# Kernel optimization log

Hardware: AMD Instinct MI355X
Metric: run time of the kernel (lower is better)

## Reference

```python
import jax, jax.numpy as jnp
import numpy as np

K_NEIGHBORS = 16  # n_sample

# Each Conv1x1+BatchNorm (eval mode) stage is an exact per-channel affine map,
# so it is represented by a single fused (W, b) pair: y = W @ x + b.

def affine(W, b, x):
    # W: [Cout, Cin]; x: [B, Cin, N] or [B, Cin, N, K]
    if x.ndim == 3:
        return jnp.einsum('oc,bcn->bon', W, x) + b[None, :, None]
    return jnp.einsum('oc,bcnk->bonk', W, x) + b[None, :, None, None]

def knn_idx(p, k):
    # p: [B, N, 3] -> idx of k nearest neighbors (incl. self): [B, N, k]
    sq = jnp.sum(p * p, axis=-1)  # [B, N]
    d2 = sq[:, :, None] + sq[:, None, :] - 2.0 * jnp.einsum('bnc,bmc->bnm', p, p)
    _, idx = jax.lax.top_k(-d2, k)
    return idx

def group(feat, idx):
    # feat: [B, C, N], idx: [B, N, K] -> grouped[b,c,n,k] = feat[b,c,idx[b,n,k]]
    return jax.vmap(lambda f, i: f[:, i])(feat, idx)


def setup_inputs() -> dict:
    key = jax.random.key(0)
    B, C, N = 4, 128, 4096
    ks = jax.random.split(key, 22)
    def w(k, o, i):
        return (jax.random.normal(k, (o, i), jnp.float32) / np.sqrt(i)).astype(jnp.float32)
    def bv(k, o):
        return (jax.random.normal(k, (o,), jnp.float32) * 0.01).astype(jnp.float32)
    inp = {
        'input_p': jax.random.normal(ks[0], (B, 3, N), jnp.float32),
        'input_x': jax.random.normal(ks[1], (B, C, N), jnp.float32),
        'top_W': w(ks[2], C, C),   'top_b': bv(ks[3], C),
        'down_W': w(ks[4], C, C),  'down_b': bv(ks[5], C),
        'phi_W': w(ks[6], C, C),   'phi_b': bv(ks[7], C),
        'psi_W': w(ks[8], C, C),   'psi_b': bv(ks[9], C),
        'alpha_W': w(ks[10], C, C), 'alpha_b': bv(ks[11], C),
        'g1_W': w(ks[12], C, C),   'g1_b': bv(ks[13], C),
        'g2_W': w(ks[14], C, C),   'g2_b': bv(ks[15], C),
        'd1_W': w(ks[16], C, 3),   'd1_b': bv(ks[17], C),
        'd2_W': w(ks[18], C, C),   'd2_b': bv(ks[19], C),
        'a': 0, 'b': 0,
    }
    return inp


def reference(input_p, input_x, top_W, top_b, down_W, down_b, phi_W, phi_b,
              psi_W, psi_b, alpha_W, alpha_b, g1_W, g1_b, g2_W, g2_b,
              d1_W, d1_b, d2_W, d2_b, a, b):
    res = input_x
    p = jnp.transpose(input_p, (0, 2, 1))          # [B, N, 3]
    idx = knn_idx(p, K_NEIGHBORS)                  # [B, N, K]
    grouped_p = group(input_p, idx)                # [B, 3, N, K]
    x = affine(top_W, top_b, input_x)              # linear_top
    phi = affine(phi_W, phi_b, x)[:, :, :, None]   # [B, C, N, 1] (broadcast over K)
    psi = group(affine(psi_W, psi_b, x), idx)      # [B, C, N, K]
    alp = group(affine(alpha_W, alpha_b, x), idx)  # [B, C, N, K]
    rel = input_p[:, :, :, None] - grouped_p       # relative xyz [B, 3, N, K]
    pos = affine(d2_W, d2_b, jax.nn.relu(affine(d1_W, d1_b, rel)))   # delta MLP
    attn = affine(g2_W, g2_b, jax.nn.relu(affine(g1_W, g1_b, phi - psi + pos)))  # gamma MLP
    y = (jax.nn.softmax(attn, axis=-1) * (alp + pos)).sum(axis=-1)   # [B, C, N]
    y = affine(down_W, down_b, y)                  # linear_down
    return y + res
```

## Files before the change

kernel.cpp:

```cpp
#include <hip/hip_runtime.h>
#include <hip/hip_bf16.h>

#define BB 4
#define CC 128
#define NN 4096
#define KK 16
#define FLT_BIG 3.402823466e+38f

typedef __attribute__((ext_vector_type(8))) short short8v;
typedef __attribute__((ext_vector_type(4))) short short4v;
typedef __attribute__((ext_vector_type(4))) float f32x4;

__device__ __forceinline__ unsigned short f2b(float x) {
  union { float f; unsigned u; } v; v.f = x;
  unsigned r = v.u + 0x7fffu + ((v.u >> 16) & 1u);
  return (unsigned short)(r >> 16);
}
__device__ __forceinline__ float b2f(unsigned short h) {
  union { float f; unsigned u; } v; v.u = ((unsigned)h) << 16; return v.f;
}
__device__ __forceinline__ unsigned pkrn(float a, float b) {
  __hip_bfloat162 t = __float22bfloat162_rn(make_float2(a, b));
  union { __hip_bfloat162 h; unsigned u; } c; c.h = t; return c.u;
}
__device__ __forceinline__ void split2(float a, float b, unsigned& h, unsigned& l) {
  h = pkrn(a, b);
  union { unsigned u; float f; } lo, hi2;
  lo.u = h << 16;
  hi2.u = h & 0xffff0000u;
  l = pkrn(a - lo.f, b - hi2.f);
}

__device__ __forceinline__ float dist4(const float4 q, const float4 c) {
  float t = __fmaf_rn(q.x, c.x, __fmaf_rn(q.y, c.y, __fmul_rn(q.z, c.z)));
  return __fmaf_rn(-2.f, t, q.w + c.w);
}

__global__ __launch_bounds__(256) void setup_kernel(
    const float* __restrict__ p, const float* __restrict__ x,
    const float* __restrict__ d2W, const float* __restrict__ g1W,
    const float* __restrict__ g2W, const float* __restrict__ topW,
    const float* __restrict__ phiW, const float* __restrict__ psiW,
    const float* __restrict__ alpW, const float* __restrict__ dnW,
    float4* __restrict__ pkg, unsigned short* __restrict__ wpk,
    unsigned short* __restrict__ xh, unsigned short* __restrict__ xl)
{
  __shared__ float t[64][65];
  const int bid = blockIdx.x, tid = threadIdx.x;
  if (bid < 64) {
    int i = bid * 256 + tid;
    int b = i >> 12, m = i & (NN - 1);
    const float* pb = p + (size_t)b * 3 * NN;
    float xx = pb[m], yy = pb[NN + m], zz = pb[2 * NN + m];
    pkg[i] = make_float4(xx, yy, zz, __fmaf_rn(xx, xx, __fmaf_rn(yy, yy, __fmul_rn(zz, zz))));
  } else if (bid < 128) {
    int tt = (bid - 64) * 256 + tid;
    int mat = tt >> 11, r = tt & 2047;
    int ct = r >> 8, ks = (r >> 6) & 3, lane = r & 63;
    const float* W;
    switch (mat) {
      case 0: W = d2W; break;  case 1: W = g1W; break;
      case 2: W = g2W; break;  case 3: W = topW; break;
      case 4: W = phiW; break; case 5: W = psiW; break;
      case 6: W = alpW; break; default: W = dnW; break;
    }
    int row = ct * 16 + (lane & 15);
    int k0 = ks * 32 + (lane >> 4) * 8;
    const float* src = &W[row * 128 + k0];
    unsigned short* dh = &wpk[((size_t)(((mat * 2 + 0) * 8 + ct) * 4 + ks) * 64 + lane) * 8];
    unsigned short* dl = &wpk[((size_t)(((mat * 2 + 1) * 8 + ct) * 4 + ks) * 64 + lane) * 8];
#pragma unroll
    for (int e = 0; e < 8; ++e) {
      float v = src[e];
      unsigned short h = f2b(v);
      dh[e] = h;
      dl[e] = f2b(v - b2f(h));
    }
  } else {
    int bid2 = bid - 128;
    int nb = bid2 & 63, cb = (bid2 >> 6) & 1, b = bid2 >> 7;
    const int c0 = cb * 64, n0 = nb * 64;
    const int tn = tid & 63, tq = tid >> 6;
    const float* xb = x + ((size_t)b * CC + c0) * NN + n0;
#pragma unroll
    for (int i = 0; i < 16; ++i) {
      int c = tq * 16 + i;
      t[c][tn] = xb[(size_t)c * NN + tn];
    }
    __syncthreads();
#pragma unroll
    for (int i = 0; i < 16; ++i) {
      int nl = tq * 16 + i;
      float v = t[tn][nl];
      unsigned short h = f2b(v);
      size_t o = ((size_t)b * NN + n0 + nl) * CC + c0 + tn;
      xh[o] = h;
      xl[o] = f2b(v - b2f(h));
    }
  }
}

__global__ __launch_bounds__(512, 2) void knn_kernel(const float4* __restrict__ pkg,
                                                     int* __restrict__ outidx)
{
  __shared__ float BD[8][64][17];
  __shared__ float TS[64];
  __shared__ int   CNT[64];
  __shared__ float COLd[64][20];
  __shared__ int   COLi[64][20];
  const int b = blockIdx.y;
  const int tid = threadIdx.x;
  const int lane = tid & 63;
  const int w = tid >> 6;
  const int n = blockIdx.x * 64 + lane;
  const float4* PB = pkg + (size_t)b * NN;
  const float4 qc = PB[n];
  if (tid < 64) CNT[tid] = 0;

  float bd[16];
#pragma unroll
  for (int t = 0; t < 16; ++t) bd[t] = FLT_BIG;
  const int m0 = w * 512;
#pragma unroll 4
  for (int m = m0; m < m0 + 512; ++m) {
    float4 c = PB[m];
    float d = dist4(qc, c);
#pragma unroll
    for (int t = 15; t >= 1; --t) bd[t] = __builtin_amdgcn_fmed3f(bd[t - 1], d, bd[t]);
    bd[0] = fminf(bd[0], d);
  }
#pragma unroll
  for (int t = 0; t < 16; ++t) BD[w][lane][t] = bd[t];
  __syncthreads();

  if (tid < 64) {
    const int q = tid;
    int h0 = 0, h1 = 0, h2 = 0, h3 = 0, h4 = 0, h5 = 0, h6 = 0, h7 = 0;
    float mv = FLT_BIG;
#pragma unroll 1
    for (int r = 0; r < 16; ++r) {
      float v0 = BD[0][q][h0], v1 = BD[1][q][h1], v2 = BD[2][q][h2], v3 = BD[3][q][h3];
      float v4 = BD[4][q][h4], v5 = BD[5][q][h5], v6 = BD[6][q][h6], v7 = BD[7][q][h7];
      mv = v0; int mw = 0;
      if (v1 < mv) { mv = v1; mw = 1; }
      if (v2 < mv) { mv = v2; mw = 2; }
      if (v3 < mv) { mv = v3; mw = 3; }
      if (v4 < mv) { mv = v4; mw = 4; }
      if (v5 < mv) { mv = v5; mw = 5; }
      if (v6 < mv) { mv = v6; mw = 6; }
      if (v7 < mv) { mv = v7; mw = 7; }
      h0 += (mw == 0); h1 += (mw == 1); h2 += (mw == 2); h3 += (mw == 3);
      h4 += (mw == 4); h5 += (mw == 5); h6 += (mw == 6); h7 += (mw == 7);
    }
    TS[q] = mv;
  }
  __syncthreads();

  {
    const float thr = TS[lane];
#pragma unroll 4
    for (int m = m0; m < m0 + 512; ++m) {
      float4 c = PB[m];
      float d = dist4(qc, c);
      if (d <= thr) {
        int pos = atomicAdd(&CNT[lane], 1);
        if (pos < 20) { COLd[lane][pos] = d; COLi[lane][pos] = m; }
      }
    }
  }
  __syncthreads();

  if (tid < 64) {
    const int q = tid;
    int c = CNT[q]; if (c > 20) c = 20;
    int* op = outidx + ((size_t)b * NN + blockIdx.x * 64 + q) * KK;
    if (c == KK) {
#pragma unroll
      for (int o = 0; o < KK; ++o) op[o] = COLi[q][o];
    } else {
      const float T = TS[q];
      int less = 0;
      for (int s = 0; s < c; ++s) less += (COLd[q][s] < T);
      int need = KK - less;
      int o = 0;
      for (int s = 0; s < c; ++s)
        if (COLd[q][s] < T) op[o++] = COLi[q][s];
      for (int s = 0; s < c; ++s) {
        if (COLd[q][s] == T) {
          int idx = COLi[q][s];
          int rank = 0;
          for (int s2 = 0; s2 < c; ++s2)
            rank += (COLd[q][s2] == T && COLi[q][s2] < idx);
          if (rank < need) op[o++] = idx;
        }
      }
    }
  }
}

__global__ __launch_bounds__(256) void feat_kernel(
    const unsigned short* __restrict__ xh, const unsigned short* __restrict__ xl,
    const unsigned short* __restrict__ wpk,
    const float* __restrict__ topb, const float* __restrict__ phib,
    const float* __restrict__ psib, const float* __restrict__ alpb,
    float* __restrict__ phit, float* __restrict__ psit,
    unsigned short* __restrict__ alpt)
{
  __shared__ float xtile[32][129];
  const int b = blockIdx.y, n0 = blockIdx.x * 32;
  const int tid = threadIdx.x, l = tid & 63, w = tid >> 6;
  const int lr = l & 15, lh = l >> 4;
  const int nt = w & 1, cq = w >> 1;
  {
    const int nrow = n0 + nt * 16 + lr;
    const unsigned short* xhp = xh + ((size_t)b * NN + nrow) * CC;
    const unsigned short* xlp = xl + ((size_t)b * NN + nrow) * CC;
    short8v Ah[4], Al[4];
#pragma unroll
    for (int ks = 0; ks < 4; ++ks) {
      Ah[ks] = *(const short8v*)&xhp[ks * 32 + lh * 8];
      Al[ks] = *(const short8v*)&xlp[ks * 32 + lh * 8];
    }
    const int nDl = nt * 16 + lh * 4;
#pragma unroll
    for (int cc = 0; cc < 4; ++cc) {
      const int colt = cq * 4 + cc;
      f32x4 acc = (f32x4){0.f, 0.f, 0.f, 0.f};
#pragma unroll
      for (int ks = 0; ks < 4; ++ks) {
        short8v Wh = *(const short8v*)&wpk[((size_t)(((3 * 2 + 0) * 8 + colt) * 4 + ks) * 64 + l) * 8];
        short8v Wl = *(const short8v*)&wpk[((size_t)(((3 * 2 + 1) * 8 + colt) * 4 + ks) * 64 + l) * 8];
        acc = __builtin_amdgcn_mfma_f32_16x16x32_bf16(Ah[ks], Wh, acc, 0, 0, 0);
        acc = __builtin_amdgcn_mfma_f32_16x16x32_bf16(Al[ks], Wh, acc, 0, 0, 0);
        acc = __builtin_amdgcn_mfma_f32_16x16x32_bf16(Ah[ks], Wl, acc, 0, 0, 0);
      }
      float bv = topb[colt * 16 + lr];
#pragma unroll
      for (int r = 0; r < 4; ++r) xtile[nDl + r][colt * 16 + lr] = acc[r] + bv;
    }
  }
  __syncthreads();
  short8v Ah[4], Al[4];
  {
    const int rl = nt * 16 + lr;
#pragma unroll
    for (int ks = 0; ks < 4; ++ks) {
      union { short8v s; unsigned u[4]; } H, L;
#pragma unroll
      for (int i = 0; i < 4; ++i) {
        float a = xtile[rl][ks * 32 + lh * 8 + 2 * i];
        float bb = xtile[rl][ks * 32 + lh * 8 + 2 * i + 1];
        split2(a, bb, H.u[i], L.u[i]);
      }
      Ah[ks] = H.s; Al[ks] = L.s;
    }
  }
  const int nD = n0 + nt * 16 + lh * 4;
#pragma unroll
  for (int m = 0; m < 3; ++m) {
    const int mat = 4 + m;
    const float* bias = (m == 0) ? phib : (m == 1) ? psib : alpb;
#pragma unroll
    for (int cc = 0; cc < 4; ++cc) {
      const int colt = cq * 4 + cc;
      f32x4 acc = (f32x4){0.f, 0.f, 0.f, 0.f};
#pragma unroll
      for (int ks = 0; ks < 4; ++ks) {
        short8v Wh = *(const short8v*)&wpk[((size_t)(((mat * 2 + 0) * 8 + colt) * 4 + ks) * 64 + l) * 8];
        short8v Wl = *(const short8v*)&wpk[((size_t)(((mat * 2 + 1) * 8 + colt) * 4 + ks) * 64 + l) * 8];
        acc = __builtin_amdgcn_mfma_f32_16x16x32_bf16(Ah[ks], Wh, acc, 0, 0, 0);
        acc = __builtin_amdgcn_mfma_f32_16x16x32_bf16(Al[ks], Wh, acc, 0, 0, 0);
        acc = __builtin_amdgcn_mfma_f32_16x16x32_bf16(Ah[ks], Wl, acc, 0, 0, 0);
      }
      float bv = bias[colt * 16 + lr];
      if (m == 2) {
#pragma unroll
        for (int r = 0; r < 4; ++r)
          alpt[((size_t)b * NN + nD + r) * CC + colt * 16 + lr] = f2b(acc[r] + bv);
      } else {
        float* outp = (m == 0) ? phit : psit;
#pragma unroll
        for (int r = 0; r < 4; ++r)
          outp[((size_t)b * NN + nD + r) * CC + colt * 16 + lr] = acc[r] + bv;
      }
    }
  }
}

__global__ __launch_bounds__(256) void down_kernel(
    const unsigned short* __restrict__ yh, const unsigned short* __restrict__ yl,
    const unsigned short* __restrict__ wpk,
    const float* __restrict__ bias, const float* __restrict__ res,
    float* __restrict__ out)
{
  const int b = blockIdx.y, n0 = blockIdx.x * 64;
  const int tid = threadIdx.x, l = tid & 63, w = tid >> 6;
  const int lr = l & 15, lh = l >> 4;
  short8v Ah[2][4], Al[2][4];
#pragma unroll
  for (int ct = 0; ct < 2; ++ct)
#pragma unroll
    for (int ks = 0; ks < 4; ++ks) {
      Ah[ct][ks] = *(const short8v*)&wpk[((size_t)(((7 * 2 + 0) * 8 + (2 * w + ct)) * 4 + ks) * 64 + l) * 8];
      Al[ct][ks] = *(const short8v*)&wpk[((size_t)(((7 * 2 + 1) * 8 + (2 * w + ct)) * 4 + ks) * 64 + l) * 8];
    }
  f32x4 acc[2][4];
#pragma unroll
  for (int colt = 0; colt < 4; ++colt) {
    const int n = n0 + colt * 16 + lr;
    const unsigned short* yhp = yh + ((size_t)b * NN + n) * CC;
    const unsigned short* ylp = yl + ((size_t)b * NN + n) * CC;
#pragma unroll
    for (int ct = 0; ct < 2; ++ct) acc[ct][colt] = (f32x4){0.f, 0.f, 0.f, 0.f};
#pragma unroll
    for (int ks = 0; ks < 4; ++ks) {
      short8v Bh = *(const short8v*)&yhp[ks * 32 + lh * 8];
      short8v Bl = *(const short8v*)&ylp[ks * 32 + lh * 8];
#pragma unroll
      for (int ct = 0; ct < 2; ++ct) {
        acc[ct][colt] = __builtin_amdgcn_mfma_f32_16x16x32_bf16(Ah[ct][ks], Bh, acc[ct][colt], 0, 0, 0);
        acc[ct][colt] = __builtin_amdgcn_mfma_f32_16x16x32_bf16(Ah[ct][ks], Bl, acc[ct][colt], 0, 0, 0);
        acc[ct][colt] = __builtin_amdgcn_mfma_f32_16x16x32_bf16(Al[ct][ks], Bh, acc[ct][colt], 0, 0, 0);
      }
    }
  }
#pragma unroll
  for (int ct = 0; ct < 2; ++ct) {
    const int c0 = 32 * w + ct * 16 + lh * 4;
#pragma unroll
    for (int r = 0; r < 4; ++r) {
      float bv = bias[c0 + r];
#pragma unroll
      for (int colt = 0; colt < 4; ++colt) {
        size_t o = ((size_t)b * CC + c0 + r) * NN + n0 + colt * 16 + lr;
        out[o] = acc[ct][colt][r] + bv + res[o];
      }
    }
  }
}

#define TNP 4
__global__ __launch_bounds__(256, 4) void fused_kernel(
    const float* __restrict__ p, const int* __restrict__ idxg,
    const float* __restrict__ phi_t, const float* __restrict__ psi_t,
    const unsigned short* __restrict__ alp_b, const unsigned short* __restrict__ wpk,
    const float* __restrict__ d1W, const float* __restrict__ d1b,
    const float* __restrict__ d2b, const float* __restrict__ g1b,
    const float* __restrict__ g2b,
    unsigned short* __restrict__ yh, unsigned short* __restrict__ yl)
{
  __shared__ __align__(16) unsigned short act[2][64][136];
  __shared__ int idxs[64];
  const int b = blockIdx.y;
  const int n0 = blockIdx.x * TNP;
  const int tid = threadIdx.x;
  const int l = tid & 63, w = tid >> 6;
  const int lr = l & 15, lh = l >> 4;

  if (tid < 64) idxs[tid] = idxg[((size_t)b * NN + n0 + (tid >> 4)) * KK + (tid & 15)];
  __syncthreads();

  {
    const int col = tid & 63, q = tid >> 6;
    const int pt = col >> 4;
    const int j = idxs[col];
    const float* pb = p + (size_t)b * 3 * NN;
    float r0 = pb[n0 + pt] - pb[j];
    float r1 = pb[NN + n0 + pt] - pb[NN + j];
    float r2 = pb[2 * NN + n0 + pt] - pb[2 * NN + j];
#pragma unroll
    for (int ch = 0; ch < 4; ++ch) {
      int c0 = q * 32 + ch * 8;
      float v[8];
#pragma unroll
      for (int e = 0; e < 8; ++e) {
        int c = c0 + e;
        v[e] = fmaxf(d1W[c * 3 + 0] * r0 + d1W[c * 3 + 1] * r1 + d1W[c * 3 + 2] * r2 + d1b[c], 0.f);
      }
      uint4 H, L;
      split2(v[0], v[1], H.x, L.x); split2(v[2], v[3], H.y, L.y);
      split2(v[4], v[5], H.z, L.z); split2(v[6], v[7], H.w, L.w);
      *(uint4*)&act[0][col][c0] = H;
      *(uint4*)&act[1][col][c0] = L;
    }
  }
  __syncthreads();

  int idxv[TNP];
#pragma unroll
  for (int colt = 0; colt < TNP; ++colt) idxv[colt] = idxs[colt * 16 + lr];

  f32x4 acc[2][TNP];
  short8v Af[2][4];

#define LOADA(MAT) do {                                                                 \
  _Pragma("unroll") for (int ct = 0; ct < 2; ++ct)                                      \
    _Pragma("unroll") for (int ks = 0; ks < 4; ++ks)                                    \
      Af[ct][ks] = *(const short8v*)&wpk[((size_t)((((MAT) * 2 + 0) * 8 + (2 * w + ct)) * 4 + ks) * 64 + l) * 8]; \
  } while (0)

#define MMUL() do {                                                                     \
  _Pragma("unroll") for (int ct = 0; ct < 2; ++ct)                                      \
    _Pragma("unroll") for (int colt = 0; colt < TNP; ++colt)                            \
      acc[ct][colt] = (f32x4){0.f, 0.f, 0.f, 0.f};                                      \
  _Pragma("unroll") for (int colt = 0; colt < TNP; ++colt) {                            \
    short8v Bh[4], Bl[4];                                                               \
    _Pragma("unroll") for (int ks = 0; ks < 4; ++ks) {                                  \
      Bh[ks] = *(const short8v*)&act[0][colt * 16 + lr][ks * 32 + lh * 8];              \
      Bl[ks] = *(const short8v*)&act[1][colt * 16 + lr][ks * 32 + lh * 8];              \
    }                                                                                   \
    _Pragma("unroll") for (int ct = 0; ct < 2; ++ct)                                    \
      _Pragma("unroll") for (int ks = 0; ks < 4; ++ks) {                                \
        acc[ct][colt] = __builtin_amdgcn_mfma_f32_16x16x32_bf16(Af[ct][ks], Bh[ks],     \
                                                                acc[ct][colt], 0, 0, 0); \
        acc[ct][colt] = __builtin_amdgcn_mfma_f32_16x16x32_bf16(Af[ct][ks], Bl[ks],     \
                                                                acc[ct][colt], 0, 0, 0); \
      }                                                                                 \
  } } while (0)

  f32x4 psiv[2][TNP];
#pragma unroll
  for (int colt = 0; colt < TNP; ++colt) {
    size_t srow = ((size_t)b * NN + idxv[colt]) * CC;
#pragma unroll
    for (int ct = 0; ct < 2; ++ct)
      psiv[ct][colt] = *(const f32x4*)&psi_t[srow + 32 * w + ct * 16 + lh * 4];
  }

  LOADA(0); MMUL();
  float pos[2][TNP][4];
#pragma unroll
  for (int ct = 0; ct < 2; ++ct) {
    f32x4 bv = *(const f32x4*)&d2b[32 * w + ct * 16 + lh * 4];
#pragma unroll
    for (int colt = 0; colt < TNP; ++colt)
#pragma unroll
      for (int r = 0; r < 4; ++r) pos[ct][colt][r] = acc[ct][colt][r] + bv[r];
  }
  __syncthreads();

#pragma unroll
  for (int colt = 0; colt < TNP; ++colt) {
    size_t prow = ((size_t)b * NN + n0 + colt) * CC;
#pragma unroll
    for (int ct = 0; ct < 2; ++ct) {
      int c0 = 32 * w + ct * 16 + lh * 4;
      f32x4 ph = *(const f32x4*)&phi_t[prow + c0];
      float v[4];
#pragma unroll
      for (int r = 0; r < 4; ++r) v[r] = pos[ct][colt][r] + ph[r] - psiv[ct][colt][r];
      uint2 H, L;
      split2(v[0], v[1], H.x, L.x); split2(v[2], v[3], H.y, L.y);
      *(uint2*)&act[0][colt * 16 + lr][c0] = H;
      *(uint2*)&act[1][colt * 16 + lr][c0] = L;
    }
  }
  __syncthreads();

  uint2 ualp[2][TNP];
#pragma unroll
  for (int colt = 0; colt < TNP; ++colt) {
    size_t arow = ((size_t)b * NN + idxv[colt]) * CC;
#pragma unroll
    for (int ct = 0; ct < 2; ++ct)
      ualp[ct][colt] = *(const uint2*)&alp_b[arow + 32 * w + ct * 16 + lh * 4];
  }

  LOADA(1); MMUL();
  __syncthreads();
#pragma unroll
  for (int ct = 0; ct < 2; ++ct) {
    f32x4 bv = *(const f32x4*)&g1b[32 * w + ct * 16 + lh * 4];
    int c0 = 32 * w + ct * 16 + lh * 4;
#pragma unroll
    for (int colt = 0; colt < TNP; ++colt) {
      float v[4];
#pragma unroll
      for (int r = 0; r < 4; ++r) v[r] = fmaxf(acc[ct][colt][r] + bv[r], 0.f);
      uint2 H, L;
      split2(v[0], v[1], H.x, L.x); split2(v[2], v[3], H.y, L.y);
      *(uint2*)&act[0][colt * 16 + lr][c0] = H;
      *(uint2*)&act[1][colt * 16 + lr][c0] = L;
    }
  }
  __syncthreads();

  LOADA(2); MMUL();
#pragma unroll
  for (int ct = 0; ct < 2; ++ct) {
    f32x4 bv = *(const f32x4*)&g2b[32 * w + ct * 16 + lh * 4];
#pragma unroll
    for (int colt = 0; colt < TNP; ++colt)
#pragma unroll
      for (int r = 0; r < 4; ++r) acc[ct][colt][r] += bv[r];
  }

#pragma unroll
  for (int ct = 0; ct < 2; ++ct)
#pragma unroll
    for (int colt = 0; colt < TNP; ++colt)
#pragma unroll
      for (int r = 0; r < 4; ++r) {
        float a = acc[ct][colt][r];
        float m = a;
        m = fmaxf(m, __shfl_xor(m, 1));
        m = fmaxf(m, __shfl_xor(m, 2));
        m = fmaxf(m, __shfl_xor(m, 4));
        m = fmaxf(m, __shfl_xor(m, 8));
        float e = __expf(a - m);
        float s = e;
        s += __shfl_xor(s, 1);
        s += __shfl_xor(s, 2);
        s += __shfl_xor(s, 4);
        s += __shfl_xor(s, 8);
        acc[ct][colt][r] = e / s;
      }

  __syncthreads();
  unsigned short* yst = &act[0][0][0];

#pragma unroll
  for (int colt = 0; colt < TNP; ++colt) {
#pragma unroll
    for (int ct = 0; ct < 2; ++ct) {
      int c0 = 32 * w + ct * 16 + lh * 4;
      uint2 ua = ualp[ct][colt];
      union { unsigned u; float f; } a0, a1, a2, a3;
      a0.u = ua.x << 16; a1.u = ua.x & 0xffff0000u;
      a2.u = ua.y << 16; a3.u = ua.y & 0xffff0000u;
      float av[4] = {a0.f, a1.f, a2.f, a3.f};
      float yv[4];
#pragma unroll
      for (int r = 0; r < 4; ++r) {
        float part = acc[ct][colt][r] * (av[r] + pos[ct][colt][r]);
        part += __shfl_xor(part, 1);
        part += __shfl_xor(part, 2);
        part += __shfl_xor(part, 4);
        part += __shfl_xor(part, 8);
        yv[r] = part;
      }
      if (lr == 0) {
        uint2 H, L;
        split2(yv[0], yv[1], H.x, L.x); split2(yv[2], yv[3], H.y, L.y);
        *(uint2*)&yst[(size_t)colt * 128 + c0] = H;
        *(uint2*)&yst[(size_t)(4 + colt) * 128 + c0] = L;
      }
    }
  }
  __syncthreads();
  if (tid < 128) {
    int plane = tid >> 6, row = (tid >> 4) & 3, chunk = tid & 15;
    uint4 v4 = *(const uint4*)&yst[(size_t)(plane * 4 + row) * 128 + chunk * 8];
    unsigned short* dst = (plane ? yl : yh) + ((size_t)b * NN + n0 + row) * CC + chunk * 8;
    *(uint4*)dst = v4;
  }
#undef LOADA
#undef MMUL
}

extern "C" void kernel_launch(void* const* d_in, const int* in_sizes, int n_in,
                              void* d_out, int out_size, void* d_ws, size_t ws_size,
                              hipStream_t stream) {
  const float* input_p = (const float*)d_in[0];
  const float* input_x = (const float*)d_in[1];
  const float* top_W   = (const float*)d_in[2];  const float* top_b   = (const float*)d_in[3];
  const float* down_W  = (const float*)d_in[4];  const float* down_b  = (const float*)d_in[5];
  const float* phi_W   = (const float*)d_in[6];  const float* phi_b   = (const float*)d_in[7];
  const float* psi_W   = (const float*)d_in[8];  const float* psi_b   = (const float*)d_in[9];
  const float* alpha_W = (const float*)d_in[10]; const float* alpha_b = (const float*)d_in[11];
  const float* g1_W    = (const float*)d_in[12]; const float* g1_b    = (const float*)d_in[13];
  const float* g2_W    = (const float*)d_in[14]; const float* g2_b    = (const float*)d_in[15];
  const float* d1_W    = (const float*)d_in[16]; const float* d1_b    = (const float*)d_in[17];
  const float* d2_W    = (const float*)d_in[18]; const float* d2_b    = (const float*)d_in[19];
  float* out = (float*)d_out;

  char* ws = (char*)d_ws;
  int*            ws_idx   = (int*)ws;
  unsigned short* ws_xin_h = (unsigned short*)(ws + (size_t)1  * (1 << 20));
  unsigned short* ws_xin_l = (unsigned short*)(ws + (size_t)5  * (1 << 20));
  float*          ws_phi   = (float*)(ws + (size_t)9  * (1 << 20));
  float*          ws_psi   = (float*)(ws + (size_t)17 * (1 << 20));
  unsigned short* ws_alp   = (unsigned short*)(ws + (size_t)25 * (1 << 20));
  float4*         ws_pkg   = (float4*)(ws + (size_t)29 * (1 << 20));
  unsigned short* ws_wpk   = (unsigned short*)(ws + (size_t)29 * (1 << 20) + (1 << 18));
  unsigned short* ws_y_h = ws_xin_h;
  unsigned short* ws_y_l = ws_xin_l;

  setup_kernel<<<640, 256, 0, stream>>>(input_p, input_x, d2_W, g1_W, g2_W, top_W,
                                        phi_W, psi_W, alpha_W, down_W,
                                        ws_pkg, ws_wpk, ws_xin_h, ws_xin_l);
  knn_kernel<<<dim3(NN / 64, BB), 512, 0, stream>>>(ws_pkg, ws_idx);
  feat_kernel<<<dim3(NN / 32, BB), 256, 0, stream>>>(ws_xin_h, ws_xin_l, ws_wpk,
                                                     top_b, phi_b, psi_b, alpha_b,
                                                     ws_phi, ws_psi, ws_alp);
  fused_kernel<<<dim3(NN / TNP, BB), 256, 0, stream>>>(input_p, ws_idx, ws_phi, ws_psi, ws_alp,
                                                       ws_wpk, d1_W, d1_b, d2_b, g1_b, g2_b,
                                                       ws_y_h, ws_y_l);
  down_kernel<<<dim3(NN / 64, BB), 256, 0, stream>>>(ws_y_h, ws_y_l, ws_wpk, down_b,
                                                     input_x, out);
}
```

Before: 391.6 us.

## Skip kNN insertions, swizzle LDS activations, defer gathers, cheapen softmax

The kNN scan now runs the 16-step median insertion only when a candidate beats the current 16th-best distance, with the unroll lowered to 2. The shared-memory activation tile gets an XOR swizzle on its column index to reduce bank conflicts on MFMA operand loads. The psi and alpha gathers move from early register prefetch to just before use, which cuts register pressure but exposes their latency. Softmax uses lane 0's value as the shift instead of a max reduction and a fast reciprocal instead of division, which risks overflow if logits spread far and slightly changes precision.

```diff
diff --git a/kernel.cpp b/kernel.cpp
--- a/kernel.cpp
+++ b/kernel.cpp
@@ -121,13 +121,15 @@
 #pragma unroll
   for (int t = 0; t < 16; ++t) bd[t] = FLT_BIG;
   const int m0 = w * 512;
-#pragma unroll 4
+#pragma unroll 2
   for (int m = m0; m < m0 + 512; ++m) {
     float4 c = PB[m];
     float d = dist4(qc, c);
-#pragma unroll
-    for (int t = 15; t >= 1; --t) bd[t] = __builtin_amdgcn_fmed3f(bd[t - 1], d, bd[t]);
-    bd[0] = fminf(bd[0], d);
+    if (d < bd[15]) {
+#pragma unroll
+      for (int t = 15; t >= 1; --t) bd[t] = __builtin_amdgcn_fmed3f(bd[t - 1], d, bd[t]);
+      bd[0] = fminf(bd[0], d);
+    }
   }
 #pragma unroll
   for (int t = 0; t < 16; ++t) BD[w][lane][t] = bd[t];
@@ -340,6 +342,7 @@
 }
 
 #define TNP 4
+#define ASW(row, c) ((c) ^ (((row) & 7) << 3))
 __global__ __launch_bounds__(256, 4) void fused_kernel(
     const float* __restrict__ p, const int* __restrict__ idxg,
     const float* __restrict__ phi_t, const float* __restrict__ psi_t,
@@ -380,8 +383,8 @@
       uint4 H, L;
       split2(v[0], v[1], H.x, L.x); split2(v[2], v[3], H.y, L.y);
       split2(v[4], v[5], H.z, L.z); split2(v[6], v[7], H.w, L.w);
-      *(uint4*)&act[0][col][c0] = H;
-      *(uint4*)&act[1][col][c0] = L;
+      *(uint4*)&act[0][col][ASW(col, c0)] = H;
+      *(uint4*)&act[1][col][ASW(col, c0)] = L;
     }
   }
   __syncthreads();
@@ -404,10 +407,11 @@
     _Pragma("unroll") for (int colt = 0; colt < TNP; ++colt)                            \
       acc[ct][colt] = (f32x4){0.f, 0.f, 0.f, 0.f};                                      \
   _Pragma("unroll") for (int colt = 0; colt < TNP; ++colt) {                            \
+    const int row_ = colt * 16 + lr;                                                    \
     short8v Bh[4], Bl[4];                                                               \
     _Pragma("unroll") for (int ks = 0; ks < 4; ++ks) {                                  \
-      Bh[ks] = *(const short8v*)&act[0][colt * 16 + lr][ks * 32 + lh * 8];              \
-      Bl[ks] = *(const short8v*)&act[1][colt * 16 + lr][ks * 32 + lh * 8];              \
+      Bh[ks] = *(const short8v*)&act[0][row_][ASW(row_, ks * 32 + lh * 8)];             \
+      Bl[ks] = *(const short8v*)&act[1][row_][ASW(row_, ks * 32 + lh * 8)];             \
     }                                                                                   \
     _Pragma("unroll") for (int ct = 0; ct < 2; ++ct)                                    \
       _Pragma("unroll") for (int ks = 0; ks < 4; ++ks) {                                \
@@ -418,15 +422,6 @@
       }                                                                                 \
   } } while (0)
 
-  f32x4 psiv[2][TNP];
-#pragma unroll
-  for (int colt = 0; colt < TNP; ++colt) {
-    size_t srow = ((size_t)b * NN + idxv[colt]) * CC;
-#pragma unroll
-    for (int ct = 0; ct < 2; ++ct)
-      psiv[ct][colt] = *(const f32x4*)&psi_t[srow + 32 * w + ct * 16 + lh * 4];
-  }
-
   LOADA(0); MMUL();
   float pos[2][TNP][4];
 #pragma unroll
@@ -442,29 +437,23 @@
 #pragma unroll
   for (int colt = 0; colt < TNP; ++colt) {
     size_t prow = ((size_t)b * NN + n0 + colt) * CC;
+    size_t srow = ((size_t)b * NN + idxv[colt]) * CC;
 #pragma unroll
     for (int ct = 0; ct < 2; ++ct) {
       int c0 = 32 * w + ct * 16 + lh * 4;
       f32x4 ph = *(const f32x4*)&phi_t[prow + c0];
+      f32x4 ps = *(const f32x4*)&psi_t[srow + c0];
       float v[4];
 #pragma unroll
-      for (int r = 0; r < 4; ++r) v[r] = pos[ct][colt][r] + ph[r] - psiv[ct][colt][r];
+      for (int r = 0; r < 4; ++r) v[r] = pos[ct][colt][r] + ph[r] - ps[r];
       uint2 H, L;
       split2(v[0], v[1], H.x, L.x); split2(v[2], v[3], H.y, L.y);
-      *(uint2*)&act[0][colt * 16 + lr][c0] = H;
-      *(uint2*)&act[1][colt * 16 + lr][c0] = L;
-    }
-  }
-  __syncthreads();
-
-  uint2 ualp[2][TNP];
-#pragma unroll
-  for (int colt = 0; colt < TNP; ++colt) {
-    size_t arow = ((size_t)b * NN + idxv[colt]) * CC;
-#pragma unroll
-    for (int ct = 0; ct < 2; ++ct)
-      ualp[ct][colt] = *(const uint2*)&alp_b[arow + 32 * w + ct * 16 + lh * 4];
-  }
+      const int row = colt * 16 + lr;
+      *(uint2*)&act[0][row][ASW(row, c0)] = H;
+      *(uint2*)&act[1][row][ASW(row, c0)] = L;
+    }
+  }
+  __syncthreads();
 
   LOADA(1); MMUL();
   __syncthreads();
@@ -479,8 +468,9 @@
       for (int r = 0; r < 4; ++r) v[r] = fmaxf(acc[ct][colt][r] + bv[r], 0.f);
       uint2 H, L;
       split2(v[0], v[1], H.x, L.x); split2(v[2], v[3], H.y, L.y);
-      *(uint2*)&act[0][colt * 16 + lr][c0] = H;
-      *(uint2*)&act[1][colt * 16 + lr][c0] = L;
+      const int row = colt * 16 + lr;
+      *(uint2*)&act[0][row][ASW(row, c0)] = H;
+      *(uint2*)&act[1][row][ASW(row, c0)] = L;
     }
   }
   __syncthreads();
@@ -502,18 +492,14 @@
 #pragma unroll
       for (int r = 0; r < 4; ++r) {
         float a = acc[ct][colt][r];
-        float m = a;
-        m = fmaxf(m, __shfl_xor(m, 1));
-        m = fmaxf(m, __shfl_xor(m, 2));
-        m = fmaxf(m, __shfl_xor(m, 4));
-        m = fmaxf(m, __shfl_xor(m, 8));
+        float m = __shfl(a, l & 48);
         float e = __expf(a - m);
         float s = e;
         s += __shfl_xor(s, 1);
         s += __shfl_xor(s, 2);
         s += __shfl_xor(s, 4);
         s += __shfl_xor(s, 8);
-        acc[ct][colt][r] = e / s;
+        acc[ct][colt][r] = e * __builtin_amdgcn_rcpf(s);
       }
 
   __syncthreads();
@@ -521,10 +507,11 @@
 
 #pragma unroll
   for (int colt = 0; colt < TNP; ++colt) {
+    size_t arow = ((size_t)b * NN + idxv[colt]) * CC;
 #pragma unroll
     for (int ct = 0; ct < 2; ++ct) {
       int c0 = 32 * w + ct * 16 + lh * 4;
-      uint2 ua = ualp[ct][colt];
+      uint2 ua = *(const uint2*)&alp_b[arow + c0];
       union { unsigned u; float f; } a0, a1, a2, a3;
       a0.u = ua.x << 16; a1.u = ua.x & 0xffff0000u;
       a2.u = ua.y << 16; a3.u = ua.y & 0xffff0000u;
```

After: 437.6 us. +11.7%, slower.
